# Performance work log

Measured on AMD Instinct MI355X. Metric: run time of the kernel, lower is better.

The kernel has to match this reference:

```python
import jax, jax.numpy as jnp
import numpy as np


def setup_inputs() -> dict:
    key = jax.random.key(0)
    k1, k2, k3, k4 = jax.random.split(key, 4)
    B, T, E, H = 4, 2048, 1024, 16
    hs = E // H
    x = jax.random.normal(k1, (B, T, E), dtype=jnp.float32)
    # per-head projection weights (nn.Linear bias=False, stored as [H, E, head_size])
    s = 1.0 / np.sqrt(E)
    Wq = jax.random.uniform(k2, (H, E, hs), dtype=jnp.float32, minval=-s, maxval=s)
    Wk = jax.random.uniform(k3, (H, E, hs), dtype=jnp.float32, minval=-s, maxval=s)
    Wv = jax.random.uniform(k4, (H, E, hs), dtype=jnp.float32, minval=-s, maxval=s)
    return {"x": x, "Wq": Wq, "Wk": Wk, "Wv": Wv}


def reference(x, Wq, Wk, Wv):
    # x: [B, T, E]; Wq/Wk/Wv: [H, E, hs]
    B, T, E = x.shape
    H = Wq.shape[0]
    q = jnp.einsum('bte,hed->bhtd', x, Wq)
    k = jnp.einsum('bte,hed->bhtd', x, Wk)
    v = jnp.einsum('bte,hed->bhtd', x, Wv)
    scores = jnp.einsum('bhtd,bhsd->bhts', q, k)
    # causal mask applied before scaling (matches original; -inf unaffected by scale)
    causal = jnp.tril(jnp.ones((T, T), dtype=bool))
    scores = jnp.where(causal, scores, -jnp.inf)
    # NOTE: original scales by sqrt(embed_size), not sqrt(head_size)
    scores = scores / jnp.sqrt(jnp.asarray(E, dtype=scores.dtype))
    w = jax.nn.softmax(scores, axis=-1)
    # dropout: eval mode (identity)
    out = jnp.einsum('bhts,bhsd->bhtd', w, v)  # [B,H,T,hs]
    out = jnp.transpose(out, (0, 2, 1, 3)).reshape(B, T, -1)  # concat heads
    return out
```

## Files before the change

### kernel.cpp

```cpp
#include <hip/hip_runtime.h>
#include <cstdint>
#include <cmath>


typedef __attribute__((ext_vector_type(8))) __bf16 bf16x8;
typedef __attribute__((ext_vector_type(4))) __bf16 bf16x4;
typedef __attribute__((ext_vector_type(4))) float f32x4;
typedef __attribute__((ext_vector_type(16))) float f32x16;

#define B_ 4
#define T_ 2048
#define E_ 1024
#define H_ 16
#define HS_ 64

__device__ __forceinline__ f32x4 mfma16(bf16x8 a, bf16x8 b, f32x4 c) {
  return __builtin_amdgcn_mfma_f32_16x16x32_bf16(a, b, c, 0, 0, 0);
}
__device__ __forceinline__ f32x16 mfma32(bf16x8 a, bf16x8 b, f32x16 c) {
  return __builtin_amdgcn_mfma_f32_32x32x16_bf16(a, b, c, 0, 0, 0);
}

__device__ __forceinline__ void gload_lds16(const void* g, void* l) {
  __builtin_amdgcn_global_load_lds(
      (const __attribute__((address_space(1))) unsigned int*)g,
      (__attribute__((address_space(3))) unsigned int*)l,
      16, 0, 0);
}

__device__ __forceinline__ unsigned cvt_pk_bf16(float lo, float hi) {
  unsigned r;
  asm("v_cvt_pk_bf16_f32 %0, %1, %2" : "=v"(r) : "v"(lo), "v"(hi));
  return r;
}
__device__ __forceinline__ void pl32swap(unsigned& a, unsigned& b) {
  asm("v_permlane32_swap_b32 %0, %1" : "+v"(a), "+v"(b));
}

__global__ __launch_bounds__(256) void cvt_x_kernel(const float* __restrict__ x,
                                                    __bf16* __restrict__ xb) {
  int i = (blockIdx.x * 256 + threadIdx.x) * 4;
  float4 v = *(const float4*)(x + i);
  bf16x4 o;
  o[0] = (__bf16)v.x; o[1] = (__bf16)v.y; o[2] = (__bf16)v.z; o[3] = (__bf16)v.w;
  *(bf16x4*)(xb + i) = o;
}

__global__ __launch_bounds__(256) void cvt_w_kernel(const float* __restrict__ Wq,
                                                    const float* __restrict__ Wk,
                                                    const float* __restrict__ Wv,
                                                    __bf16* __restrict__ wt) {
  __shared__ float tile[64][65];
  const int e0 = blockIdx.x * 64;
  const int h = blockIdx.y;
  const int qkv = blockIdx.z;
  const int t = threadIdx.x;
  const float* W = (qkv == 0) ? Wq : (qkv == 1) ? Wk : Wv;
#pragma unroll
  for (int j = 0; j < 16; ++j) {
    int idx = j * 256 + t;
    int e = idx >> 6, d = idx & 63;
    tile[d][e] = W[((size_t)(h * 1024 + e0 + e)) * 64 + d];
  }
  __syncthreads();
#pragma unroll
  for (int j = 0; j < 16; ++j) {
    int idx = j * 256 + t;
    int d = idx >> 6, e = idx & 63;
    wt[((size_t)qkv << 20) + (size_t)(h * 64 + d) * 1024 + e0 + e] =
        (__bf16)tile[d][e];
  }
}

__global__ __launch_bounds__(256) void qkv_gemm_kernel(
    const __bf16* __restrict__ Xb, const __bf16* __restrict__ Wt,
    __bf16* __restrict__ Qb, __bf16* __restrict__ Kb, __bf16* __restrict__ Vt) {
  __shared__ __bf16 As[128 * 32];
  __shared__ __bf16 Bs[128 * 32];
  const int qkv = blockIdx.z;
  const int m0 = blockIdx.x * 128;
  const int n0 = blockIdx.y * 128;
  const int t = threadIdx.x;
  const int lane = t & 63;
  const int w = t >> 6, wr = w >> 1, wc = w & 1;
  const int g = lane >> 4, c = lane & 15;

  const __bf16* wsrc = Wt + ((size_t)qkv << 20);
  f32x4 acc[4][4] = {};

  const __bf16* ga0 = Xb + (size_t)(m0 + (t >> 2)) * 1024 + (t & 3) * 8;
  const __bf16* ga1 = Xb + (size_t)(m0 + 64 + (t >> 2)) * 1024 + (t & 3) * 8;
  const __bf16* gb0 = wsrc + (size_t)(n0 + (t >> 2)) * 1024 + (t & 3) * 8;
  const __bf16* gb1 = wsrc + (size_t)(n0 + 64 + (t >> 2)) * 1024 + (t & 3) * 8;

  for (int k0 = 0; k0 < 1024; k0 += 32) {
    __syncthreads();
    gload_lds16(ga0 + k0, &As[t * 8]);
    gload_lds16(ga1 + k0, &As[2048 + t * 8]);
    gload_lds16(gb0 + k0, &Bs[t * 8]);
    gload_lds16(gb1 + k0, &Bs[2048 + t * 8]);
    __syncthreads();

    bf16x8 af[4], bfr[4];
#pragma unroll
    for (int mi = 0; mi < 4; ++mi)
      af[mi] = *(const bf16x8*)&As[(wr * 64 + mi * 16 + c) * 32 + g * 8];
#pragma unroll
    for (int ni = 0; ni < 4; ++ni)
      bfr[ni] = *(const bf16x8*)&Bs[(wc * 64 + ni * 16 + c) * 32 + g * 8];
#pragma unroll
    for (int mi = 0; mi < 4; ++mi)
#pragma unroll
      for (int ni = 0; ni < 4; ++ni)
        acc[mi][ni] = mfma16(af[mi], bfr[ni], acc[mi][ni]);
  }

  const int mbase = m0 + wr * 64 + g * 4;
  const int nbase = n0 + wc * 64 + c;
  if (qkv < 2) {
    __bf16* dst = (qkv == 0) ? Qb : Kb;
#pragma unroll
    for (int mi = 0; mi < 4; ++mi) {
#pragma unroll
      for (int ni = 0; ni < 4; ++ni) {
        int n = nbase + ni * 16;
        int h = n >> 6, d = n & 63;
#pragma unroll
        for (int r = 0; r < 4; ++r) {
          int m = mbase + mi * 16 + r;
          int b = m >> 11, tt = m & 2047;
          dst[(((size_t)b * H_ + h) * T_ + tt) * HS_ + d] = (__bf16)acc[mi][ni][r];
        }
      }
    }
  } else {
#pragma unroll
    for (int mi = 0; mi < 4; ++mi) {
      int m = mbase + mi * 16;
      int b = m >> 11, tt = m & 2047;
#pragma unroll
      for (int ni = 0; ni < 4; ++ni) {
        int n = nbase + ni * 16;
        int h = n >> 6, d = n & 63;
        bf16x4 pk;
        pk[0] = (__bf16)acc[mi][ni][0];
        pk[1] = (__bf16)acc[mi][ni][1];
        pk[2] = (__bf16)acc[mi][ni][2];
        pk[3] = (__bf16)acc[mi][ni][3];
        *(bf16x4*)&Vt[(((size_t)b * H_ + h) * HS_ + d) * T_ + tt] = pk;
      }
    }
  }
}

__global__ __launch_bounds__(512) void attn_kernel(
    const __bf16* __restrict__ Qb, const __bf16* __restrict__ Kb,
    const __bf16* __restrict__ Vt, float* __restrict__ out) {
  __shared__ __bf16 Ks[2][64 * 64];
  __shared__ __bf16 Vs[2][64 * 64];

  const int j = blockIdx.x;
  const int bh = (j & 7) + 8 * (j >> 5);
  const int qp = (j >> 3) & 3;
  const int b = bh >> 4, hh = bh & 15;
  const int t = threadIdx.x;
  const int lane = t & 63, w = t >> 6;
  const int lr = lane & 31, h = lane >> 5;

  const __bf16* Qg = Qb + (size_t)bh * T_ * HS_;
  const __bf16* Kg = Kb + (size_t)bh * T_ * HS_;
  const __bf16* Vg = Vt + (size_t)bh * HS_ * T_;

  const int srow = t >> 3;
  const int scb = ((t & 7) << 4) ^ ((srow & 7) << 4);
  const int kxor = (lr & 7) << 4;

  const float C2 = 0.04508422f;

#pragma unroll 1
  for (int ph = 0; ph < 2; ++ph) {
    const int qt = (ph == 0) ? qp : 7 - qp;
    const int qbase = qt * 256;
    const int NT = (qt + 1) * 4;
    const int tqg = qbase + w * 32 + lr;

    const __bf16* Qrow = Qg + (size_t)(qbase + w * 32 + lr) * 64;
    bf16x8 qf0 = *(const bf16x8*)(Qrow + h * 8);
    bf16x8 qf1 = *(const bf16x8*)(Qrow + 16 + h * 8);
    bf16x8 qf2 = *(const bf16x8*)(Qrow + 32 + h * 8);
    bf16x8 qf3 = *(const bf16x8*)(Qrow + 48 + h * 8);

    f32x16 o0 = {}, o1 = {};
    float m_run = -INFINITY, l_run = 0.f;
    int cur = 0;

    gload_lds16((const char*)Kg + (size_t)srow * 128 + scb, (char*)&Ks[0][0] + t * 16);
    gload_lds16((const char*)Vg + (size_t)srow * 4096 + scb, (char*)&Vs[0][0] + t * 16);
    __syncthreads();

#pragma unroll 1
    for (int kt = 0; kt < NT; ++kt) {
      const int kbase = kt * 64;
      if (kt + 1 < NT) {
        const int nb = cur ^ 1;
        gload_lds16((const char*)Kg + (size_t)(kbase + 64 + srow) * 128 + scb,
                    (char*)&Ks[nb][0] + t * 16);
        gload_lds16((const char*)Vg + (size_t)srow * 4096 + (size_t)(kbase + 64) * 2 + scb,
                    (char*)&Vs[nb][0] + t * 16);
      }
      if (kbase <= qbase + w * 32 + 31) {
        const char* KsB = (const char*)&Ks[cur][0];
        const char* VsB = (const char*)&Vs[cur][0];

        f32x16 s0 = {}, s1 = {};
#pragma unroll
        for (int ds = 0; ds < 4; ++ds) {
          bf16x8 k0 = *(const bf16x8*)(KsB + ((lr * 128 + ds * 32 + h * 16) ^ kxor));
          bf16x8 k1 = *(const bf16x8*)(KsB + (((lr + 32) * 128 + ds * 32 + h * 16) ^ kxor));
          bf16x8 qd = (ds == 0) ? qf0 : (ds == 1) ? qf1 : (ds == 2) ? qf2 : qf3;
          s0 = mfma32(k0, qd, s0);
          s1 = mfma32(k1, qd, s1);
        }

        if (kbase + 63 > qbase + w * 32) {
#pragma unroll
          for (int r = 0; r < 16; ++r) {
            int tk0 = kbase + (r & 3) + 8 * (r >> 2) + 4 * h;
            if (tk0 > tqg) s0[r] = -INFINITY;
            if (tk0 + 32 > tqg) s1[r] = -INFINITY;
          }
        }

        float mx = s0[0];
#pragma unroll
        for (int r = 1; r < 16; ++r) mx = fmaxf(mx, s0[r]);
#pragma unroll
        for (int r = 0; r < 16; ++r) mx = fmaxf(mx, s1[r]);
        mx = fmaxf(mx, __shfl_xor(mx, 32));
        float mn = fmaxf(m_run, mx);
        float fac = __builtin_amdgcn_exp2f((m_run - mn) * C2);
        float sum = 0.f;
#pragma unroll
        for (int r = 0; r < 16; ++r) {
          s0[r] = __builtin_amdgcn_exp2f((s0[r] - mn) * C2);
          s1[r] = __builtin_amdgcn_exp2f((s1[r] - mn) * C2);
          sum += s0[r] + s1[r];
        }
        sum += __shfl_xor(sum, 32);
        l_run = l_run * fac + sum;
        m_run = mn;
#pragma unroll
        for (int r = 0; r < 16; ++r) { o0[r] *= fac; o1[r] *= fac; }

#pragma unroll
        for (int blk = 0; blk < 4; ++blk) {
          f32x16& sv = (blk < 2) ? s0 : s1;
          const int off = (blk & 1) * 8;
          unsigned u0 = cvt_pk_bf16(sv[off + 0], sv[off + 1]);
          unsigned u1 = cvt_pk_bf16(sv[off + 2], sv[off + 3]);
          unsigned u2 = cvt_pk_bf16(sv[off + 4], sv[off + 5]);
          unsigned u3 = cvt_pk_bf16(sv[off + 6], sv[off + 7]);
          pl32swap(u0, u2);
          pl32swap(u1, u3);
          union { unsigned u[4]; bf16x8 v; } pb;
          pb.u[0] = u0; pb.u[1] = u1; pb.u[2] = u2; pb.u[3] = u3;
          bf16x8 v0 = *(const bf16x8*)(VsB + ((lr * 128 + blk * 32 + h * 16) ^ kxor));
          bf16x8 v1 = *(const bf16x8*)(VsB + (((lr + 32) * 128 + blk * 32 + h * 16) ^ kxor));
          o0 = mfma32(v0, pb.v, o0);
          o1 = mfma32(v1, pb.v, o1);
        }
      }
      __syncthreads();
      cur ^= 1;
    }

    const float inv_l = 1.0f / l_run;
    float* orow = out + ((size_t)b * T_ + tqg) * E_ + hh * 64;
#pragma unroll
    for (int d0i = 0; d0i < 2; ++d0i) {
#pragma unroll
      for (int qd = 0; qd < 4; ++qd) {
        float4 v;
        const f32x16& ac = d0i ? o1 : o0;
        v.x = ac[qd * 4 + 0] * inv_l;
        v.y = ac[qd * 4 + 1] * inv_l;
        v.z = ac[qd * 4 + 2] * inv_l;
        v.w = ac[qd * 4 + 3] * inv_l;
        *(float4*)(orow + d0i * 32 + qd * 8 + 4 * h) = v;
      }
    }
  }
}

extern "C" void kernel_launch(void* const* d_in, const int* in_sizes, int n_in,
                              void* d_out, int out_size, void* d_ws, size_t ws_size,
                              hipStream_t stream) {
  const float* x = (const float*)d_in[0];
  const float* Wq = (const float*)d_in[1];
  const float* Wk = (const float*)d_in[2];
  const float* Wv = (const float*)d_in[3];
  float* out = (float*)d_out;

  char* ws = (char*)d_ws;
  __bf16* Xb = (__bf16*)ws;
  __bf16* Wt = (__bf16*)(ws + (16u << 20));
  __bf16* Qb = (__bf16*)(ws + (22u << 20));
  __bf16* Kb = (__bf16*)(ws + (38u << 20));
  __bf16* Vt = (__bf16*)(ws + (54u << 20));

  cvt_x_kernel<<<8192, 256, 0, stream>>>(x, Xb);
  cvt_w_kernel<<<dim3(16, 16, 3), 256, 0, stream>>>(Wq, Wk, Wv, Wt);
  qkv_gemm_kernel<<<dim3(64, 8, 3), 256, 0, stream>>>(Xb, Wt, Qb, Kb, Vt);
  attn_kernel<<<dim3(256), 512, 0, stream>>>(Qb, Kb, Vt, out);
}
```

Baseline: 221.4 us.

## Pipeline QKV GEMM with 4-stage LDS ring, vectorize weight convert, split attention blocks

The QKV GEMM moves from a single-buffered, twice-synchronised K loop to a 4-deep LDS ring with explicit vmcnt waits, swizzled LDS columns and raised MFMA priority, so global loads overlap compute and bank conflicts drop. The weight conversion kernel switches to float4 loads and bf16x8 stores. Attention goes from 256 blocks doing two paired causal tiles each to 512 blocks doing one tile each, scheduled largest first. It also adds a lazy softmax rescale that skips the rescale when the max grows by a bounded amount. The larger LDS footprint may lower GEMM occupancy, and the lazy rescale relies on exp2 staying within range.

```diff
diff --git a/kernel.cpp b/kernel.cpp
--- a/kernel.cpp
+++ b/kernel.cpp
@@ -57,26 +57,32 @@
   const int t = threadIdx.x;
   const float* W = (qkv == 0) ? Wq : (qkv == 1) ? Wk : Wv;
 #pragma unroll
-  for (int j = 0; j < 16; ++j) {
+  for (int j = 0; j < 4; ++j) {
     int idx = j * 256 + t;
-    int e = idx >> 6, d = idx & 63;
-    tile[d][e] = W[((size_t)(h * 1024 + e0 + e)) * 64 + d];
+    int d4 = idx & 15, e = idx >> 4;
+    float4 v = *(const float4*)&W[((size_t)(h * 1024 + e0 + e)) * 64 + d4 * 4];
+    tile[d4 * 4 + 0][e] = v.x;
+    tile[d4 * 4 + 1][e] = v.y;
+    tile[d4 * 4 + 2][e] = v.z;
+    tile[d4 * 4 + 3][e] = v.w;
   }
   __syncthreads();
 #pragma unroll
-  for (int j = 0; j < 16; ++j) {
+  for (int j = 0; j < 2; ++j) {
     int idx = j * 256 + t;
-    int d = idx >> 6, e = idx & 63;
-    wt[((size_t)qkv << 20) + (size_t)(h * 64 + d) * 1024 + e0 + e] =
-        (__bf16)tile[d][e];
+    int e8 = idx & 7, d = idx >> 3;
+    bf16x8 o;
+#pragma unroll
+    for (int i = 0; i < 8; ++i) o[i] = (__bf16)tile[d][e8 * 8 + i];
+    *(bf16x8*)&wt[((size_t)qkv << 20) + (size_t)(h * 64 + d) * 1024 + e0 + e8 * 8] = o;
   }
 }
 
 __global__ __launch_bounds__(256) void qkv_gemm_kernel(
     const __bf16* __restrict__ Xb, const __bf16* __restrict__ Wt,
     __bf16* __restrict__ Qb, __bf16* __restrict__ Kb, __bf16* __restrict__ Vt) {
-  __shared__ __bf16 As[128 * 32];
-  __shared__ __bf16 Bs[128 * 32];
+  __shared__ __bf16 As[4][128 * 32];
+  __shared__ __bf16 Bs[4][128 * 32];
   const int qkv = blockIdx.z;
   const int m0 = blockIdx.x * 128;
   const int n0 = blockIdx.y * 128;
@@ -88,31 +94,56 @@
   const __bf16* wsrc = Wt + ((size_t)qkv << 20);
   f32x4 acc[4][4] = {};
 
-  const __bf16* ga0 = Xb + (size_t)(m0 + (t >> 2)) * 1024 + (t & 3) * 8;
-  const __bf16* ga1 = Xb + (size_t)(m0 + 64 + (t >> 2)) * 1024 + (t & 3) * 8;
-  const __bf16* gb0 = wsrc + (size_t)(n0 + (t >> 2)) * 1024 + (t & 3) * 8;
-  const __bf16* gb1 = wsrc + (size_t)(n0 + 64 + (t >> 2)) * 1024 + (t & 3) * 8;
-
-  for (int k0 = 0; k0 < 1024; k0 += 32) {
-    __syncthreads();
-    gload_lds16(ga0 + k0, &As[t * 8]);
-    gload_lds16(ga1 + k0, &As[2048 + t * 8]);
-    gload_lds16(gb0 + k0, &Bs[t * 8]);
-    gload_lds16(gb1 + k0, &Bs[2048 + t * 8]);
-    __syncthreads();
-
+  const int srow = t >> 2;
+  const int cs8 = (((t & 3) ^ (srow & 3)) << 3);
+  const __bf16* gA0 = Xb + (size_t)(m0 + srow) * 1024 + cs8;
+  const __bf16* gA1 = Xb + (size_t)(m0 + 64 + srow) * 1024 + cs8;
+  const __bf16* gB0 = wsrc + (size_t)(n0 + srow) * 1024 + cs8;
+  const __bf16* gB1 = wsrc + (size_t)(n0 + 64 + srow) * 1024 + cs8;
+
+  auto stage = [&](int s) {
+    const int b = s & 3;
+    const int ko = s * 32;
+    gload_lds16(gA0 + ko, &As[b][t * 8]);
+    gload_lds16(gA1 + ko, &As[b][2048 + t * 8]);
+    gload_lds16(gB0 + ko, &Bs[b][t * 8]);
+    gload_lds16(gB1 + ko, &Bs[b][2048 + t * 8]);
+  };
+
+  stage(0); stage(1); stage(2);
+
+  const int gx = (g ^ (c & 3)) << 3;
+
+#pragma unroll 1
+  for (int kt = 0; kt < 32; ++kt) {
+    if (kt <= 29) {
+      asm volatile("s_waitcnt vmcnt(8)" ::: "memory");
+    } else if (kt == 30) {
+      asm volatile("s_waitcnt vmcnt(4)" ::: "memory");
+    } else {
+      asm volatile("s_waitcnt vmcnt(0)" ::: "memory");
+    }
+    __builtin_amdgcn_sched_barrier(0);
+    __builtin_amdgcn_s_barrier();
+    if (kt + 3 < 32) stage(kt + 3);
+
+    const __bf16* Ab = &As[kt & 3][0];
+    const __bf16* Bb = &Bs[kt & 3][0];
     bf16x8 af[4], bfr[4];
 #pragma unroll
     for (int mi = 0; mi < 4; ++mi)
-      af[mi] = *(const bf16x8*)&As[(wr * 64 + mi * 16 + c) * 32 + g * 8];
+      af[mi] = *(const bf16x8*)&Ab[(wr * 64 + mi * 16 + c) * 32 + gx];
 #pragma unroll
     for (int ni = 0; ni < 4; ++ni)
-      bfr[ni] = *(const bf16x8*)&Bs[(wc * 64 + ni * 16 + c) * 32 + g * 8];
+      bfr[ni] = *(const bf16x8*)&Bb[(wc * 64 + ni * 16 + c) * 32 + gx];
+    __builtin_amdgcn_s_setprio(1);
 #pragma unroll
     for (int mi = 0; mi < 4; ++mi)
 #pragma unroll
       for (int ni = 0; ni < 4; ++ni)
         acc[mi][ni] = mfma16(af[mi], bfr[ni], acc[mi][ni]);
+    __builtin_amdgcn_s_setprio(0);
+    __builtin_amdgcn_sched_barrier(0);
   }
 
   const int mbase = m0 + wr * 64 + g * 4;
@@ -160,8 +191,9 @@
   __shared__ __bf16 Vs[2][64 * 64];
 
   const int j = blockIdx.x;
-  const int bh = (j & 7) + 8 * (j >> 5);
-  const int qp = (j >> 3) & 3;
+  const int g8 = j >> 6;
+  const int qt = (g8 < 4) ? (7 - g8) : (g8 - 4);
+  const int bh = j & 63;
   const int b = bh >> 4, hh = bh & 15;
   const int t = threadIdx.x;
   const int lane = t & 63, w = t >> 6;
@@ -177,117 +209,120 @@
 
   const float C2 = 0.04508422f;
 
+  const int qbase = qt * 256;
+  const int NT = (qt + 1) * 4;
+  const int tqg = qbase + w * 32 + lr;
+
+  const __bf16* Qrow = Qg + (size_t)tqg * 64;
+  bf16x8 qf0 = *(const bf16x8*)(Qrow + h * 8);
+  bf16x8 qf1 = *(const bf16x8*)(Qrow + 16 + h * 8);
+  bf16x8 qf2 = *(const bf16x8*)(Qrow + 32 + h * 8);
+  bf16x8 qf3 = *(const bf16x8*)(Qrow + 48 + h * 8);
+
+  f32x16 o0 = {}, o1 = {};
+  float m_run = -INFINITY, l_run = 0.f;
+  int cur = 0;
+
+  gload_lds16((const char*)Kg + (size_t)srow * 128 + scb, (char*)&Ks[0][0] + t * 16);
+  gload_lds16((const char*)Vg + (size_t)srow * 4096 + scb, (char*)&Vs[0][0] + t * 16);
+  __syncthreads();
+
 #pragma unroll 1
-  for (int ph = 0; ph < 2; ++ph) {
-    const int qt = (ph == 0) ? qp : 7 - qp;
-    const int qbase = qt * 256;
-    const int NT = (qt + 1) * 4;
-    const int tqg = qbase + w * 32 + lr;
-
-    const __bf16* Qrow = Qg + (size_t)(qbase + w * 32 + lr) * 64;
-    bf16x8 qf0 = *(const bf16x8*)(Qrow + h * 8);
-    bf16x8 qf1 = *(const bf16x8*)(Qrow + 16 + h * 8);
-    bf16x8 qf2 = *(const bf16x8*)(Qrow + 32 + h * 8);
-    bf16x8 qf3 = *(const bf16x8*)(Qrow + 48 + h * 8);
-
-    f32x16 o0 = {}, o1 = {};
-    float m_run = -INFINITY, l_run = 0.f;
-    int cur = 0;
-
-    gload_lds16((const char*)Kg + (size_t)srow * 128 + scb, (char*)&Ks[0][0] + t * 16);
-    gload_lds16((const char*)Vg + (size_t)srow * 4096 + scb, (char*)&Vs[0][0] + t * 16);
-    __syncthreads();
-
-#pragma unroll 1
-    for (int kt = 0; kt < NT; ++kt) {
-      const int kbase = kt * 64;
-      if (kt + 1 < NT) {
-        const int nb = cur ^ 1;
-        gload_lds16((const char*)Kg + (size_t)(kbase + 64 + srow) * 128 + scb,
-                    (char*)&Ks[nb][0] + t * 16);
-        gload_lds16((const char*)Vg + (size_t)srow * 4096 + (size_t)(kbase + 64) * 2 + scb,
-                    (char*)&Vs[nb][0] + t * 16);
-      }
-      if (kbase <= qbase + w * 32 + 31) {
-        const char* KsB = (const char*)&Ks[cur][0];
-        const char* VsB = (const char*)&Vs[cur][0];
-
-        f32x16 s0 = {}, s1 = {};
-#pragma unroll
-        for (int ds = 0; ds < 4; ++ds) {
-          bf16x8 k0 = *(const bf16x8*)(KsB + ((lr * 128 + ds * 32 + h * 16) ^ kxor));
-          bf16x8 k1 = *(const bf16x8*)(KsB + (((lr + 32) * 128 + ds * 32 + h * 16) ^ kxor));
-          bf16x8 qd = (ds == 0) ? qf0 : (ds == 1) ? qf1 : (ds == 2) ? qf2 : qf3;
-          s0 = mfma32(k0, qd, s0);
-          s1 = mfma32(k1, qd, s1);
+  for (int kt = 0; kt < NT; ++kt) {
+    const int kbase = kt * 64;
+    if (kt + 1 < NT) {
+      const int nb = cur ^ 1;
+      gload_lds16((const char*)Kg + (size_t)(kbase + 64 + srow) * 128 + scb,
+                  (char*)&Ks[nb][0] + t * 16);
+      gload_lds16((const char*)Vg + (size_t)srow * 4096 + (size_t)(kbase + 64) * 2 + scb,
+                  (char*)&Vs[nb][0] + t * 16);
+    }
+    if (kbase <= qbase + w * 32 + 31) {
+      const char* KsB = (const char*)&Ks[cur][0];
+      const char* VsB = (const char*)&Vs[cur][0];
+
+      f32x16 s0 = {}, s1 = {};
+      __builtin_amdgcn_s_setprio(1);
+#pragma unroll
+      for (int ds = 0; ds < 4; ++ds) {
+        bf16x8 k0 = *(const bf16x8*)(KsB + ((lr * 128 + ds * 32 + h * 16) ^ kxor));
+        bf16x8 k1 = *(const bf16x8*)(KsB + (((lr + 32) * 128 + ds * 32 + h * 16) ^ kxor));
+        bf16x8 qd = (ds == 0) ? qf0 : (ds == 1) ? qf1 : (ds == 2) ? qf2 : qf3;
+        s0 = mfma32(k0, qd, s0);
+        s1 = mfma32(k1, qd, s1);
+      }
+      __builtin_amdgcn_s_setprio(0);
+
+      if (kbase + 63 > qbase + w * 32) {
+#pragma unroll
+        for (int r = 0; r < 16; ++r) {
+          int tk0 = kbase + (r & 3) + 8 * (r >> 2) + 4 * h;
+          if (tk0 > tqg) s0[r] = -INFINITY;
+          if (tk0 + 32 > tqg) s1[r] = -INFINITY;
         }
-
-        if (kbase + 63 > qbase + w * 32) {
-#pragma unroll
-          for (int r = 0; r < 16; ++r) {
-            int tk0 = kbase + (r & 3) + 8 * (r >> 2) + 4 * h;
-            if (tk0 > tqg) s0[r] = -INFINITY;
-            if (tk0 + 32 > tqg) s1[r] = -INFINITY;
-          }
-        }
-
-        float mx = s0[0];
-#pragma unroll
-        for (int r = 1; r < 16; ++r) mx = fmaxf(mx, s0[r]);
-#pragma unroll
-        for (int r = 0; r < 16; ++r) mx = fmaxf(mx, s1[r]);
-        mx = fmaxf(mx, __shfl_xor(mx, 32));
+      }
+
+      float mx = s0[0];
+#pragma unroll
+      for (int r = 1; r < 16; ++r) mx = fmaxf(mx, s0[r]);
+#pragma unroll
+      for (int r = 0; r < 16; ++r) mx = fmaxf(mx, s1[r]);
+      mx = fmaxf(mx, __shfl_xor(mx, 32));
+      if (!__all(mx - m_run <= 256.f)) {
         float mn = fmaxf(m_run, mx);
         float fac = __builtin_amdgcn_exp2f((m_run - mn) * C2);
-        float sum = 0.f;
-#pragma unroll
-        for (int r = 0; r < 16; ++r) {
-          s0[r] = __builtin_amdgcn_exp2f((s0[r] - mn) * C2);
-          s1[r] = __builtin_amdgcn_exp2f((s1[r] - mn) * C2);
-          sum += s0[r] + s1[r];
-        }
-        sum += __shfl_xor(sum, 32);
-        l_run = l_run * fac + sum;
+        l_run *= fac;
+#pragma unroll
+        for (int r = 0; r < 16; ++r) { o0[r] *= fac; o1[r] *= fac; }
         m_run = mn;
-#pragma unroll
-        for (int r = 0; r < 16; ++r) { o0[r] *= fac; o1[r] *= fac; }
-
-#pragma unroll
-        for (int blk = 0; blk < 4; ++blk) {
-          f32x16& sv = (blk < 2) ? s0 : s1;
-          const int off = (blk & 1) * 8;
-          unsigned u0 = cvt_pk_bf16(sv[off + 0], sv[off + 1]);
-          unsigned u1 = cvt_pk_bf16(sv[off + 2], sv[off + 3]);
-          unsigned u2 = cvt_pk_bf16(sv[off + 4], sv[off + 5]);
-          unsigned u3 = cvt_pk_bf16(sv[off + 6], sv[off + 7]);
-          pl32swap(u0, u2);
-          pl32swap(u1, u3);
-          union { unsigned u[4]; bf16x8 v; } pb;
-          pb.u[0] = u0; pb.u[1] = u1; pb.u[2] = u2; pb.u[3] = u3;
-          bf16x8 v0 = *(const bf16x8*)(VsB + ((lr * 128 + blk * 32 + h * 16) ^ kxor));
-          bf16x8 v1 = *(const bf16x8*)(VsB + (((lr + 32) * 128 + blk * 32 + h * 16) ^ kxor));
-          o0 = mfma32(v0, pb.v, o0);
-          o1 = mfma32(v1, pb.v, o1);
-        }
-      }
-      __syncthreads();
-      cur ^= 1;
-    }
-
-    const float inv_l = 1.0f / l_run;
-    float* orow = out + ((size_t)b * T_ + tqg) * E_ + hh * 64;
-#pragma unroll
-    for (int d0i = 0; d0i < 2; ++d0i) {
-#pragma unroll
-      for (int qd = 0; qd < 4; ++qd) {
-        float4 v;
-        const f32x16& ac = d0i ? o1 : o0;
-        v.x = ac[qd * 4 + 0] * inv_l;
-        v.y = ac[qd * 4 + 1] * inv_l;
-        v.z = ac[qd * 4 + 2] * inv_l;
-        v.w = ac[qd * 4 + 3] * inv_l;
-        *(float4*)(orow + d0i * 32 + qd * 8 + 4 * h) = v;
-      }
+      }
+      float sum = 0.f;
+#pragma unroll
+      for (int r = 0; r < 16; ++r) {
+        s0[r] = __builtin_amdgcn_exp2f((s0[r] - m_run) * C2);
+        s1[r] = __builtin_amdgcn_exp2f((s1[r] - m_run) * C2);
+        sum += s0[r] + s1[r];
+      }
+      sum += __shfl_xor(sum, 32);
+      l_run += sum;
+
+      __builtin_amdgcn_s_setprio(1);
+#pragma unroll
+      for (int blk = 0; blk < 4; ++blk) {
+        f32x16& sv = (blk < 2) ? s0 : s1;
+        const int off = (blk & 1) * 8;
+        unsigned u0 = cvt_pk_bf16(sv[off + 0], sv[off + 1]);
+        unsigned u1 = cvt_pk_bf16(sv[off + 2], sv[off + 3]);
+        unsigned u2 = cvt_pk_bf16(sv[off + 4], sv[off + 5]);
+        unsigned u3 = cvt_pk_bf16(sv[off + 6], sv[off + 7]);
+        pl32swap(u0, u2);
+        pl32swap(u1, u3);
+        union { unsigned u[4]; bf16x8 v; } pb;
+        pb.u[0] = u0; pb.u[1] = u1; pb.u[2] = u2; pb.u[3] = u3;
+        bf16x8 v0 = *(const bf16x8*)(VsB + ((lr * 128 + blk * 32 + h * 16) ^ kxor));
+        bf16x8 v1 = *(const bf16x8*)(VsB + (((lr + 32) * 128 + blk * 32 + h * 16) ^ kxor));
+        o0 = mfma32(v0, pb.v, o0);
+        o1 = mfma32(v1, pb.v, o1);
+      }
+      __builtin_amdgcn_s_setprio(0);
+    }
+    __syncthreads();
+    cur ^= 1;
+  }
+
+  const float inv_l = 1.0f / l_run;
+  float* orow = out + ((size_t)b * T_ + tqg) * E_ + hh * 64;
+#pragma unroll
+  for (int d0i = 0; d0i < 2; ++d0i) {
+#pragma unroll
+    for (int qd = 0; qd < 4; ++qd) {
+      float4 v;
+      const f32x16& ac = d0i ? o1 : o0;
+      v.x = ac[qd * 4 + 0] * inv_l;
+      v.y = ac[qd * 4 + 1] * inv_l;
+      v.z = ac[qd * 4 + 2] * inv_l;
+      v.w = ac[qd * 4 + 3] * inv_l;
+      *(float4*)(orow + d0i * 32 + qd * 8 + 4 * h) = v;
     }
   }
 }
@@ -311,5 +346,5 @@
   cvt_x_kernel<<<8192, 256, 0, stream>>>(x, Xb);
   cvt_w_kernel<<<dim3(16, 16, 3), 256, 0, stream>>>(Wq, Wk, Wv, Wt);
   qkv_gemm_kernel<<<dim3(64, 8, 3), 256, 0, stream>>>(Xb, Wt, Qb, Kb, Vt);
-  attn_kernel<<<dim3(256), 512, 0, stream>>>(Qb, Kb, Vt, out);
-}
+  attn_kernel<<<dim3(512), 512, 0, stream>>>(Qb, Kb, Vt, out);
+}
```

New measurement: 225.9 us. 2.0% more time.
